# Performance work log

Hardware: AMD Instinct MI355X
Metric: run time of the kernel (lower is better)

## Reference

```python
import jax, jax.numpy as jnp
import numpy as np

H = 128            # hidden_dim
R = 16             # num_rbf
L = 3              # num_atom_encoder_layers
LAT = 32           # latent_dim
NUM_ATOM_TYPES = 64
CUTOFF = 5.0       # atom_cutoff
N_RES = 2048
DEG = 16           # avg radius-graph degree
_PATTERN = np.array([19, 20, 21, 22, 23, 24, 25, 22])  # ragged atoms/residue, mean 22


def setup_inputs() -> dict:
    key = jax.random.key(0)
    ks = jax.random.split(key, 16)
    apr = np.tile(_PATTERN, N_RES // len(_PATTERN))        # (N,) atoms per residue
    A = int(apr.sum())                                     # 45056 atoms
    E = A * DEG                                            # 720896 edges
    rng = np.random.default_rng(0)

    def gl(k, shape, fan_in):
        return jax.random.normal(k, shape, jnp.float32) * (fan_in ** -0.5)

    return {
        "atom_coords": jax.random.normal(ks[0], (A, 3), jnp.float32) * 10.0,
        "atom_types": jax.random.randint(ks[1], (A,), 0, NUM_ATOM_TYPES),
        "residue_indices": jnp.asarray(np.repeat(np.arange(N_RES), apr)),
        "residue_types": jax.random.randint(ks[2], (N_RES,), 0, 4),
        "atoms_per_residue": jnp.asarray(apr),
        "edge_src": jnp.asarray(rng.integers(0, A, E)),
        "edge_dst": jnp.asarray(rng.integers(0, A, E)),
        # learned parameters
        "atom_embed": gl(ks[3], (NUM_ATOM_TYPES, H), 1.0),
        "residue_embed": gl(ks[4], (4, H), 1.0),
        "We1": gl(ks[5], (L, 2 * H + R, H), 2 * H + R), "be1": jnp.zeros((L, H)),
        "We2": gl(ks[6], (L, H, H), H), "be2": jnp.zeros((L, H)),
        "Wh1": gl(ks[7], (L, 2 * H, H), 2 * H), "bh1": jnp.zeros((L, H)),
        "Wh2": gl(ks[8], (L, H, H), H), "bh2": jnp.zeros((L, H)),
        "Wq": gl(ks[9], (H, H), H), "bq": jnp.zeros((H,)),
        "Wk": gl(ks[10], (H, H), H), "bk": jnp.zeros((H,)),
        "Wv": gl(ks[11], (H, H), H), "bv": jnp.zeros((H,)),
        "Wmu": gl(ks[12], (H, LAT), H), "bmu": jnp.zeros((LAT,)),
        "Wlv": gl(ks[13], (H, LAT), H) * 0.01, "blv": jnp.full((LAT,), -2.0),
    }


def reference(atom_coords, atom_types, residue_indices, residue_types,
              atoms_per_residue, edge_src, edge_dst,
              atom_embed, residue_embed,
              We1, be1, We2, be2, Wh1, bh1, Wh2, bh2,
              Wq, bq, Wk, bk, Wv, bv, Wmu, bmu, Wlv, blv):
    A = atom_coords.shape[0]
    N = residue_types.shape[0]
    coords = atom_coords - atom_coords.mean(0, keepdims=True)  # center_coords

    # Gaussian radial basis expansion of edge distances
    d = jnp.linalg.norm(coords[edge_src] - coords[edge_dst], axis=-1)  # (E,)
    centers = jnp.linspace(0.0, CUTOFF, R)
    gamma = (R / CUTOFF) ** 2
    edge_attr = jnp.exp(-gamma * (d[:, None] - centers) ** 2)          # (E,R)

    # atom features: atom-type embed + residue-type embed scattered to atoms
    res_emb = residue_embed[residue_types]                             # (N,H)
    h = atom_embed[atom_types] + res_emb[residue_indices]              # (A,H)

    # EGNN layers (update_coords=False): message MLP -> sum-agg -> residual node MLP
    for l in range(L):
        m = jnp.concatenate([h[edge_src], h[edge_dst], edge_attr], axis=-1)  # (E,2H+R)
        m = jax.nn.silu(m @ We1[l] + be1[l])
        m = jax.nn.silu(m @ We2[l] + be2[l])                                  # (E,H)
        agg = jax.ops.segment_sum(m, edge_dst, num_segments=A)               # (A,H)
        u = jnp.concatenate([h, agg], axis=-1)                               # (A,2H)
        u = jax.nn.silu(u @ Wh1[l] + bh1[l])
        h = h + (u @ Wh2[l] + bh2[l])

    # segment (per-residue) attention pooling of atoms -> residues
    q = res_emb @ Wq + bq                                              # (N,H)
    k = h @ Wk + bk                                                    # (A,H)
    v = h @ Wv + bv                                                    # (A,H)
    scores = jnp.sum(q[residue_indices] * k, axis=-1) * (H ** -0.5)    # (A,)
    smax = jax.ops.segment_max(scores, residue_indices, num_segments=N)
    ex = jnp.exp(scores - smax[residue_indices])
    denom = jax.ops.segment_sum(ex, residue_indices, num_segments=N)
    w = ex / denom[residue_indices]
    pooled = jax.ops.segment_sum(w[:, None] * v, residue_indices, num_segments=N)  # (N,H)

    mu = pooled @ Wmu + bmu
    logvar = jnp.clip(pooled @ Wlv + blv, -10.0, 2.0)
    return mu, logvar
```

## Files before the change

kernel.cpp:

```cpp
#include <hip/hip_runtime.h>
#include <hip/hip_bf16.h>

#define H 128
#define LATD 32

typedef __attribute__((ext_vector_type(8))) _Float16 half8t;
typedef __attribute__((ext_vector_type(4))) _Float16 half4t;
typedef __attribute__((ext_vector_type(2))) _Float16 half2t;
typedef __attribute__((ext_vector_type(8))) unsigned short u16x8;
typedef __attribute__((ext_vector_type(4))) float f32x4;

#define OFF_RBF 0
#define OFF_W2  12288
#define OFF_PROJ 61440
#define OFF_H1  159744
#define OFF_H2  258048
#define OFF_KV  307200
#define WP_TOTAL 339968

__device__ __forceinline__ float silu_f(float x) {
  return x * __builtin_amdgcn_rcpf(1.0f + __expf(-x));
}
__device__ __forceinline__ unsigned short f16u(float x) {
  _Float16 hh = (_Float16)x;
  return *(unsigned short*)&hh;
}

__global__ void k_init_h(const float* __restrict__ atom_embed,
                         const float* __restrict__ residue_embed,
                         const int* __restrict__ atype,
                         const int* __restrict__ ridx,
                         const int* __restrict__ rtype,
                         float* __restrict__ h, unsigned short* __restrict__ hb, int A) {
  int i = blockIdx.x * blockDim.x + threadIdx.x;
  if (i >= A * H) return;
  int a = i >> 7, j = i & 127;
  float v = atom_embed[atype[a] * H + j] + residue_embed[rtype[ridx[a]] * H + j];
  h[i] = v;
  hb[i] = f16u(v);
}

__global__ void k_dist(const float* __restrict__ coords,
                       const int* __restrict__ esrc, const int* __restrict__ edst,
                       float* __restrict__ dbuf, int E) {
  int e = blockIdx.x * blockDim.x + threadIdx.x;
  if (e >= E) return;
  int s = esrc[e], t = edst[e];
  float dx = coords[3*s+0] - coords[3*t+0];
  float dy = coords[3*s+1] - coords[3*t+1];
  float dz = coords[3*s+2] - coords[3*t+2];
  dbuf[e] = sqrtf(dx*dx + dy*dy + dz*dz);
}

__global__ void k_starts(const int* __restrict__ ridx, int* __restrict__ starts, int A) {
  int a = blockIdx.x * blockDim.x + threadIdx.x;
  if (a >= A) return;
  if (a == 0 || ridx[a] != ridx[a-1]) starts[ridx[a]] = a;
}

__global__ void k_bias2(const float* __restrict__ b1, const float* __restrict__ b2,
                        float* __restrict__ bkv) {
  int t = threadIdx.x;
  bkv[t] = (t < 128) ? b1[t] : b2[t - 128];
}

__global__ void k_hist(const int* __restrict__ edst, int* __restrict__ cnt, int E) {
  int e = blockIdx.x * blockDim.x + threadIdx.x;
  if (e < E) atomicAdd(&cnt[edst[e]], 1);
}

__global__ __launch_bounds__(1024) void k_scanA(const int* __restrict__ cnt,
                                                int* __restrict__ cursor,
                                                int* __restrict__ bsum, int A) {
  __shared__ int buf[1024];
  int tid = threadIdx.x;
  int i = blockIdx.x * 1024 + tid;
  int v = (i < A) ? cnt[i] : 0;
  buf[tid] = v;
  __syncthreads();
  #pragma unroll
  for (int off = 1; off < 1024; off <<= 1) {
    int nv = (tid >= off) ? buf[tid - off] : 0;
    __syncthreads();
    buf[tid] += nv;
    __syncthreads();
  }
  if (i < A) cursor[i] = buf[tid] - v;
  if (tid == 1023) bsum[blockIdx.x] = buf[1023];
}

__global__ void k_scanB(int* __restrict__ bsum, int nb) {
  int lane = threadIdx.x;
  int v = (lane < nb) ? bsum[lane] : 0;
  int s = v;
  #pragma unroll
  for (int off = 1; off < 64; off <<= 1) {
    int nv = __shfl_up(s, off);
    if (lane >= off) s += nv;
  }
  if (lane < nb) bsum[lane] = s - v;
}

__global__ void k_scanC(int* __restrict__ cursor, const int* __restrict__ bsum, int A) {
  int i = blockIdx.x * blockDim.x + threadIdx.x;
  if (i < A) cursor[i] += bsum[i >> 10];
}

__global__ void k_scatter(const int* __restrict__ edst, int* __restrict__ cursor,
                          int* __restrict__ eperm, int E) {
  int e = blockIdx.x * blockDim.x + threadIdx.x;
  if (e >= E) return;
  int p = atomicAdd(&cursor[edst[e]], 1);
  eperm[p] = e;
}

__global__ void k_pack(const float* __restrict__ We1, const float* __restrict__ We2,
                       const float* __restrict__ Wh1, const float* __restrict__ Wh2,
                       const float* __restrict__ Wk,  const float* __restrict__ Wv,
                       unsigned short* __restrict__ wp) {
  int t = blockIdx.x * blockDim.x + threadIdx.x;
  if (t >= WP_TOTAL) return;
  if (t < OFF_W2) {
    int u = t - OFF_RBF; int layer = u / 4096, idx = u % 4096;
    int i = idx & 7, lane = (idx >> 3) & 63, ct = (idx >> 9) & 7;
    int k = ((lane >> 4) * 8) + i;
    int c = ct * 16 + (lane & 15);
    const float* src = We1 + (size_t)layer * 272 * H;
    wp[t] = f16u(k < 16 ? src[(size_t)(256 + k) * H + c] : 0.0f);
  } else if (t < OFF_PROJ) {
    int u = t - OFF_W2; int layer = u / 16384, idx = u % 16384;
    int i = idx & 7, lane = (idx >> 3) & 63, ct = (idx >> 9) & 7, kt = idx >> 12;
    int k = kt * 32 + (lane >> 4) * 8 + i, c = ct * 16 + (lane & 15);
    const float* src = We2 + (size_t)layer * 128 * H;
    wp[t] = f16u(src[(size_t)k * H + c]);
  } else if (t < OFF_H1) {
    int u = t - OFF_PROJ; int layer = u / 32768, idx = u % 32768;
    int i = idx & 7, lane = (idx >> 3) & 63, ct = (idx >> 9) & 15, kt = idx >> 13;
    int k = kt * 32 + (lane >> 4) * 8 + i, c = ct * 16 + (lane & 15);
    const float* src = We1 + (size_t)layer * 272 * H;
    float v = (c < 128) ? src[(size_t)k * H + c] : src[(size_t)(128 + k) * H + (c - 128)];
    wp[t] = f16u(v);
  } else if (t < OFF_H2) {
    int u = t - OFF_H1; int layer = u / 32768, idx = u % 32768;
    int i = idx & 7, lane = (idx >> 3) & 63, ct = (idx >> 9) & 7, kt = idx >> 12;
    int k = kt * 32 + (lane >> 4) * 8 + i, c = ct * 16 + (lane & 15);
    const float* src = Wh1 + (size_t)layer * 256 * H;
    wp[t] = f16u(src[(size_t)k * H + c]);
  } else if (t < OFF_KV) {
    int u = t - OFF_H2; int layer = u / 16384, idx = u % 16384;
    int i = idx & 7, lane = (idx >> 3) & 63, ct = (idx >> 9) & 7, kt = idx >> 12;
    int k = kt * 32 + (lane >> 4) * 8 + i, c = ct * 16 + (lane & 15);
    const float* src = Wh2 + (size_t)layer * 128 * H;
    wp[t] = f16u(src[(size_t)k * H + c]);
  } else {
    int idx = t - OFF_KV;
    int i = idx & 7, lane = (idx >> 3) & 63, ct = (idx >> 9) & 15, kt = idx >> 13;
    int k = kt * 32 + (lane >> 4) * 8 + i, c = ct * 16 + (lane & 15);
    float v = (c < 128) ? Wk[(size_t)k * H + c] : Wv[(size_t)k * H + (c - 128)];
    wp[t] = f16u(v);
  }
}

__global__ __launch_bounds__(256) void k_proj(
    const unsigned short* __restrict__ hb, const unsigned short* __restrict__ Wp,
    unsigned short* __restrict__ Ph, int A, const float* __restrict__ bias) {
  const int tid = threadIdx.x, l = tid & 63, wv = tid >> 6;
  const int lr = l & 15, lk = (l >> 4) * 8;
  const int a0 = blockIdx.x * 64;
  f32x4 acc[4][4] = {};
  #pragma unroll
  for (int kt = 0; kt < 4; ++kt) {
    half8t a[4], b[4];
    #pragma unroll
    for (int rt = 0; rt < 4; ++rt) {
      int row = a0 + rt * 16 + lr; if (row >= A) row = A - 1;
      a[rt] = *(const half8t*)&hb[(size_t)row * H + kt * 32 + lk];
    }
    #pragma unroll
    for (int ci = 0; ci < 4; ++ci)
      b[ci] = *(const half8t*)&Wp[(((size_t)kt * 16 + wv * 4 + ci) * 64 + l) * 8];
    #pragma unroll
    for (int rt = 0; rt < 4; ++rt)
      #pragma unroll
      for (int ci = 0; ci < 4; ++ci)
        acc[rt][ci] = __builtin_amdgcn_mfma_f32_16x16x32_f16(a[rt], b[ci], acc[rt][ci], 0, 0, 0);
  }
  #pragma unroll
  for (int rt = 0; rt < 4; ++rt)
    #pragma unroll
    for (int ci = 0; ci < 4; ++ci) {
      int col = (wv * 4 + ci) * 16 + lr;
      float bb = bias ? bias[col] : 0.0f;
      #pragma unroll
      for (int rr = 0; rr < 4; ++rr) {
        int row = a0 + rt * 16 + (l >> 4) * 4 + rr;
        if (row < A) Ph[(size_t)row * 256 + col] = f16u(acc[rt][ci][rr] + bb);
      }
    }
}

#define ES 136

__global__ __launch_bounds__(256) void k_edge_mfma(
    const unsigned short* __restrict__ Ph, const float* __restrict__ dbuf,
    const int* __restrict__ esrc, const int* __restrict__ edst,
    const int* __restrict__ eperm,
    const unsigned short* __restrict__ Wr, const float* __restrict__ be1,
    const unsigned short* __restrict__ W2p, const float* __restrict__ be2,
    float* __restrict__ agg, int E) {
  __shared__ __align__(16) unsigned short SH[64 * ES];
  __shared__ int dstv[64];
  __shared__ float dval[64];

  const int tid = threadIdx.x;
  const int e0 = blockIdx.x * 64;
  const int l = tid & 63, wv = tid >> 6;
  const int lr = l & 15, lk = (l >> 4) * 8, g4 = (l >> 4) * 4;
  const int ct0 = wv * 2;

  {
    const int r = tid >> 2, qt = tid & 3;
    int e = e0 + r;
    int ec = (e < E) ? e : (E - 1);
    int es = eperm[ec];
    int s = esrc[es], t = edst[es];
    if (qt == 0) {
      dstv[r] = (e < E) ? t : -1;
      dval[r] = dbuf[es];
    }
    const half8t* ps = (const half8t*)(Ph + (size_t)s * 256);
    const half8t* pt = (const half8t*)(Ph + (size_t)t * 256 + 128);
    half8t* pr = (half8t*)&SH[r * ES];
    #pragma unroll
    for (int i = 0; i < 4; ++i)
      pr[qt * 4 + i] = ps[qt * 4 + i] + pt[qt * 4 + i];
  }
  __syncthreads();

  f32x4 acc[2][4];
  #pragma unroll
  for (int cj = 0; cj < 2; ++cj) {
    int cbase = (ct0 + cj) * 16 + g4;
    #pragma unroll
    for (int et = 0; et < 4; ++et) {
      half4t p4 = *(const half4t*)&SH[(et * 16 + lr) * ES + cbase];
      acc[cj][et][0] = (float)p4[0];
      acc[cj][et][1] = (float)p4[1];
      acc[cj][et][2] = (float)p4[2];
      acc[cj][et][3] = (float)p4[3];
    }
  }
  {
    float dA[4];
    #pragma unroll
    for (int et = 0; et < 4; ++et) dA[et] = dval[et * 16 + lr];
    half8t br[4];
    if (lk < 16) {
      #pragma unroll
      for (int et = 0; et < 4; ++et) {
        float d = dA[et];
        #pragma unroll
        for (int i = 0; i < 8; ++i) {
          float dd = d - (float)(lk + i) * (5.0f / 15.0f);
          br[et][i] = (_Float16)__expf(-10.24f * dd * dd);
        }
      }
    } else {
      #pragma unroll
      for (int et = 0; et < 4; ++et)
        #pragma unroll
        for (int i = 0; i < 8; ++i) br[et][i] = (_Float16)0.0f;
    }
    half8t ar[2];
    #pragma unroll
    for (int cj = 0; cj < 2; ++cj)
      ar[cj] = *(const half8t*)&Wr[(((size_t)(ct0 + cj)) * 64 + l) * 8];
    #pragma unroll
    for (int et = 0; et < 4; ++et)
      #pragma unroll
      for (int cj = 0; cj < 2; ++cj)
        acc[cj][et] = __builtin_amdgcn_mfma_f32_16x16x32_f16(ar[cj], br[et], acc[cj][et], 0, 0, 0);
  }
  __syncthreads();

  #pragma unroll
  for (int cj = 0; cj < 2; ++cj) {
    f32x4 b1v = *(const f32x4*)&be1[(ct0 + cj) * 16 + g4];
    #pragma unroll
    for (int et = 0; et < 4; ++et) {
      half4t m4;
      #pragma unroll
      for (int rr = 0; rr < 4; ++rr)
        m4[rr] = (_Float16)silu_f(acc[cj][et][rr] + b1v[rr]);
      *(half4t*)&SH[(et * 16 + lr) * ES + (ct0 + cj) * 16 + g4] = m4;
    }
  }
  __syncthreads();

  f32x4 acc2[2][4] = {};
  #pragma unroll
  for (int kt = 0; kt < 4; ++kt) {
    half8t a2[2], b2[4];
    #pragma unroll
    for (int cj = 0; cj < 2; ++cj)
      a2[cj] = *(const half8t*)&W2p[(((size_t)kt * 8 + ct0 + cj) * 64 + l) * 8];
    #pragma unroll
    for (int et = 0; et < 4; ++et)
      b2[et] = *(const half8t*)&SH[(et * 16 + lr) * ES + kt * 32 + lk];
    #pragma unroll
    for (int cj = 0; cj < 2; ++cj)
      #pragma unroll
      for (int et = 0; et < 4; ++et)
        acc2[cj][et] = __builtin_amdgcn_mfma_f32_16x16x32_f16(a2[cj], b2[et], acc2[cj][et], 0, 0, 0);
  }
  __syncthreads();

  #pragma unroll
  for (int cj = 0; cj < 2; ++cj) {
    f32x4 b2v = *(const f32x4*)&be2[(ct0 + cj) * 16 + g4];
    #pragma unroll
    for (int et = 0; et < 4; ++et) {
      half4t m4;
      #pragma unroll
      for (int rr = 0; rr < 4; ++rr)
        m4[rr] = (_Float16)silu_f(acc2[cj][et][rr] + b2v[rr]);
      *(half4t*)&SH[(et * 16 + lr) * ES + (ct0 + cj) * 16 + g4] = m4;
    }
  }
  __syncthreads();

  {
    int cp = tid & 63, qr = tid >> 6;
    int rbeg = qr * 16, rend = rbeg + 16;
    float a0 = 0.f, a1 = 0.f;
    int prev = -1;
    for (int r = rbeg; r < rend; ++r) {
      int dv = dstv[r];
      half2t v = *(const half2t*)&SH[r * ES + cp * 2];
      if (dv != prev) {
        if (prev >= 0) {
          atomicAdd(&agg[(size_t)prev * H + cp * 2], a0);
          atomicAdd(&agg[(size_t)prev * H + cp * 2 + 1], a1);
        }
        a0 = a1 = 0.f;
        prev = dv;
      }
      if (dv >= 0) { a0 += (float)v[0]; a1 += (float)v[1]; }
    }
    if (prev >= 0) {
      atomicAdd(&agg[(size_t)prev * H + cp * 2], a0);
      atomicAdd(&agg[(size_t)prev * H + cp * 2 + 1], a1);
    }
  }
}

#define NXS 264
#define M1S 136

__global__ __launch_bounds__(256) void k_node_mfma(
    float* __restrict__ h, unsigned short* __restrict__ hb,
    const float* __restrict__ agg,
    const unsigned short* __restrict__ W1p, const float* __restrict__ bh1,
    const unsigned short* __restrict__ W2p, const float* __restrict__ bh2, int A) {
  __shared__ __align__(16) unsigned short Xs[32 * NXS];
  __shared__ __align__(16) unsigned short Us[32 * M1S];
  const int tid = threadIdx.x;
  const int a0 = blockIdx.x * 32;
  {
    const int r = tid >> 3, oct = tid & 7;
    int a = a0 + r; if (a >= A) a = A - 1;
    const u16x8* hr = (const u16x8*)(hb + (size_t)a * H);
    u16x8* xr = (u16x8*)&Xs[r * NXS];
    xr[oct * 2]     = hr[oct * 2];
    xr[oct * 2 + 1] = hr[oct * 2 + 1];
    const float4* ar = (const float4*)(agg + (size_t)a * H);
    u16x8 tmp[2];
    unsigned short* tp = (unsigned short*)tmp;
    #pragma unroll
    for (int i = 0; i < 4; ++i) {
      float4 av = ar[oct * 4 + i];
      tp[i*4+0] = f16u(av.x); tp[i*4+1] = f16u(av.y);
      tp[i*4+2] = f16u(av.z); tp[i*4+3] = f16u(av.w);
    }
    xr[16 + oct * 2]     = tmp[0];
    xr[16 + oct * 2 + 1] = tmp[1];
  }
  __syncthreads();

  const int l = tid & 63, wv = tid >> 6;
  const int lr = l & 15, lk = (l >> 4) * 8;
  const int ct0 = wv * 2;
  const int c0 = ct0 * 16 + lr, c1 = c0 + 16;
  const float b1a = bh1[c0], b1b = bh1[c1];
  const float b2a = bh2[c0], b2b = bh2[c1];

  f32x4 acc[2][2] = {};
  #pragma unroll
  for (int kt = 0; kt < 8; ++kt) {
    half8t a[2], b[2];
    #pragma unroll
    for (int rt = 0; rt < 2; ++rt)
      a[rt] = *(const half8t*)&Xs[(rt * 16 + lr) * NXS + kt * 32 + lk];
    #pragma unroll
    for (int j = 0; j < 2; ++j)
      b[j] = *(const half8t*)&W1p[(((size_t)kt * 8 + ct0 + j) * 64 + l) * 8];
    #pragma unroll
    for (int rt = 0; rt < 2; ++rt)
      #pragma unroll
      for (int j = 0; j < 2; ++j)
        acc[rt][j] = __builtin_amdgcn_mfma_f32_16x16x32_f16(a[rt], b[j], acc[rt][j], 0, 0, 0);
  }
  #pragma unroll
  for (int rt = 0; rt < 2; ++rt)
    #pragma unroll
    for (int j = 0; j < 2; ++j) {
      float bb = j ? b1b : b1a;
      int col = (ct0 + j) * 16 + lr;
      #pragma unroll
      for (int rr = 0; rr < 4; ++rr) {
        int row = rt * 16 + (l >> 4) * 4 + rr;
        Us[row * M1S + col] = f16u(silu_f(acc[rt][j][rr] + bb));
      }
    }
  __syncthreads();

  f32x4 acc2[2][2] = {};
  #pragma unroll
  for (int kt = 0; kt < 4; ++kt) {
    half8t a[2], b[2];
    #pragma unroll
    for (int rt = 0; rt < 2; ++rt)
      a[rt] = *(const half8t*)&Us[(rt * 16 + lr) * M1S + kt * 32 + lk];
    #pragma unroll
    for (int j = 0; j < 2; ++j)
      b[j] = *(const half8t*)&W2p[(((size_t)kt * 8 + ct0 + j) * 64 + l) * 8];
    #pragma unroll
    for (int rt = 0; rt < 2; ++rt)
      #pragma unroll
      for (int j = 0; j < 2; ++j)
        acc2[rt][j] = __builtin_amdgcn_mfma_f32_16x16x32_f16(a[rt], b[j], acc2[rt][j], 0, 0, 0);
  }
  #pragma unroll
  for (int rt = 0; rt < 2; ++rt)
    #pragma unroll
    for (int j = 0; j < 2; ++j) {
      float bb = j ? b2b : b2a;
      int col = (ct0 + j) * 16 + lr;
      #pragma unroll
      for (int rr = 0; rr < 4; ++rr) {
        int row = rt * 16 + (l >> 4) * 4 + rr;
        int a = a0 + row;
        if (a < A) {
          size_t off = (size_t)a * H + col;
          float nh = h[off] + acc2[rt][j][rr] + bb;
          h[off] = nh;
          hb[off] = f16u(nh);
        }
      }
    }
}

__global__ void k_q4(const float* __restrict__ residue_embed,
                     const float* __restrict__ Wq, const float* __restrict__ bq,
                     float* __restrict__ q4) {
  int i = blockIdx.x * blockDim.x + threadIdx.x;
  if (i >= 4 * H) return;
  int r = i >> 7, j = i & 127;
  const float* emb = residue_embed + (size_t)r * H;
  float s = bq[j];
  #pragma unroll 4
  for (int k = 0; k < H; ++k) s += emb[k] * Wq[(size_t)k*H + j];
  q4[i] = s;
}

__global__ __launch_bounds__(256) void k_pool(
    const float* __restrict__ q4, const int* __restrict__ rtype,
    const unsigned short* __restrict__ kv, const int* __restrict__ starts,
    const int* __restrict__ apr, float* __restrict__ pooled, int N) {
  int r = blockIdx.x * 4 + (threadIdx.x >> 6);
  if (r >= N) return;
  int lane = threadIdx.x & 63;
  int s0 = starts[r], cnt = apr[r];
  const float* qrow = q4 + (size_t)rtype[r] * H;
  float q0 = qrow[lane], q1 = qrow[64 + lane];
  float myscore = -1e30f;
  for (int i = 0; i < cnt; ++i) {
    const unsigned short* kr = kv + (size_t)(s0 + i) * 256;
    float p = q0 * (float)(*(const _Float16*)&kr[lane]) +
              q1 * (float)(*(const _Float16*)&kr[64 + lane]);
    #pragma unroll
    for (int off = 32; off; off >>= 1) p += __shfl_xor(p, off);
    if (lane == i) myscore = p * 0.08838834764831845f;
  }
  float val = (lane < cnt) ? myscore : -1e30f;
  float mx = val;
  #pragma unroll
  for (int off = 32; off; off >>= 1) mx = fmaxf(mx, __shfl_xor(mx, off));
  float ex = (lane < cnt) ? __expf(val - mx) : 0.0f;
  float sum = ex;
  #pragma unroll
  for (int off = 32; off; off >>= 1) sum += __shfl_xor(sum, off);
  float w = ex * __builtin_amdgcn_rcpf(sum);
  float p0 = 0.f, p1 = 0.f;
  for (int i = 0; i < cnt; ++i) {
    float wi = __shfl(w, i);
    const unsigned short* vr = kv + (size_t)(s0 + i) * 256 + 128;
    p0 += wi * (float)(*(const _Float16*)&vr[lane]);
    p1 += wi * (float)(*(const _Float16*)&vr[64 + lane]);
  }
  pooled[(size_t)r*H + lane] = p0;
  pooled[(size_t)r*H + 64 + lane] = p1;
}

__global__ void k_head(const float* __restrict__ pooled,
                       const float* __restrict__ Wmu, const float* __restrict__ bmu,
                       const float* __restrict__ Wlv, const float* __restrict__ blv,
                       float* __restrict__ out, int N) {
  int i = blockIdx.x * blockDim.x + threadIdx.x;
  if (i >= N * LATD) return;
  int r = i >> 5, j = i & 31;
  const float* p = pooled + (size_t)r * H;
  float smu = 0.f, slv = 0.f;
  #pragma unroll 4
  for (int k = 0; k < H; ++k) {
    float pv = p[k];
    smu += pv * Wmu[(size_t)k*LATD + j];
    slv += pv * Wlv[(size_t)k*LATD + j];
  }
  smu += bmu[j];
  slv += blv[j];
  slv = fminf(fmaxf(slv, -10.0f), 2.0f);
  out[i] = smu;
  out[(size_t)N*LATD + i] = slv;
}

extern "C" void kernel_launch(void* const* d_in, const int* in_sizes, int n_in,
                              void* d_out, int out_size, void* d_ws, size_t ws_size,
                              hipStream_t stream) {
  const float* coords        = (const float*)d_in[0];
  const int*   atype         = (const int*)d_in[1];
  const int*   ridx          = (const int*)d_in[2];
  const int*   rtype         = (const int*)d_in[3];
  const int*   apr           = (const int*)d_in[4];
  const int*   esrc          = (const int*)d_in[5];
  const int*   edst          = (const int*)d_in[6];
  const float* atom_embed    = (const float*)d_in[7];
  const float* residue_embed = (const float*)d_in[8];
  const float* We1 = (const float*)d_in[9];
  const float* be1 = (const float*)d_in[10];
  const float* We2 = (const float*)d_in[11];
  const float* be2 = (const float*)d_in[12];
  const float* Wh1 = (const float*)d_in[13];
  const float* bh1 = (const float*)d_in[14];
  const float* Wh2 = (const float*)d_in[15];
  const float* bh2 = (const float*)d_in[16];
  const float* Wq  = (const float*)d_in[17];
  const float* bq  = (const float*)d_in[18];
  const float* Wk  = (const float*)d_in[19];
  const float* bk  = (const float*)d_in[20];
  const float* Wv  = (const float*)d_in[21];
  const float* bv  = (const float*)d_in[22];
  const float* Wmu = (const float*)d_in[23];
  const float* bmu = (const float*)d_in[24];
  const float* Wlv = (const float*)d_in[25];
  const float* blv = (const float*)d_in[26];

  const int A = in_sizes[1];
  const int N = in_sizes[3];
  const int E = in_sizes[5];

  float* ws     = (float*)d_ws;
  float* h      = ws;
  float* agg    = h + (size_t)A * H;
  float* vbuf   = agg + (size_t)A * H;
  float* dbuf   = vbuf + (size_t)A * H;
  float* q4     = dbuf + (size_t)E;
  float* bkv    = q4 + 4 * H;
  float* pooled = bkv + 256;
  int*   starts = (int*)(pooled + (size_t)N * H);
  unsigned short* hbuf = (unsigned short*)(starts + N);
  int*   eperm  = (int*)(hbuf + (size_t)A * H);
  int*   cnt    = eperm + (size_t)E;
  int*   cursor = cnt + A;
  int*   bsum   = cursor + A;
  unsigned short* wp = (unsigned short*)(bsum + 64);
  unsigned short* Ph = (unsigned short*)vbuf;

  k_init_h<<<(A * H + 255) / 256, 256, 0, stream>>>(atom_embed, residue_embed,
                                                    atype, ridx, rtype, h, hbuf, A);
  k_dist<<<(E + 255) / 256, 256, 0, stream>>>(coords, esrc, edst, dbuf, E);
  k_starts<<<(A + 255) / 256, 256, 0, stream>>>(ridx, starts, A);
  k_pack<<<(WP_TOTAL + 255) / 256, 256, 0, stream>>>(We1, We2, Wh1, Wh2, Wk, Wv, wp);
  k_bias2<<<1, 256, 0, stream>>>(bk, bv, bkv);

  const int nb = (A + 1023) / 1024;
  hipMemsetAsync(cnt, 0, (size_t)A * sizeof(int), stream);
  k_hist<<<(E + 255) / 256, 256, 0, stream>>>(edst, cnt, E);
  k_scanA<<<nb, 1024, 0, stream>>>(cnt, cursor, bsum, A);
  k_scanB<<<1, 64, 0, stream>>>(bsum, nb);
  k_scanC<<<(A + 255) / 256, 256, 0, stream>>>(cursor, bsum, A);
  k_scatter<<<(E + 255) / 256, 256, 0, stream>>>(edst, cursor, eperm, E);

  for (int l = 0; l < 3; ++l) {
    hipMemsetAsync(agg, 0, (size_t)A * H * sizeof(float), stream);
    k_proj<<<(A + 63) / 64, 256, 0, stream>>>(
        hbuf, wp + OFF_PROJ + (size_t)l * 32768, Ph, A, nullptr);
    k_edge_mfma<<<(E + 63) / 64, 256, 0, stream>>>(
        Ph, dbuf, esrc, edst, eperm,
        wp + OFF_RBF + (size_t)l * 4096,  be1 + (size_t)l * H,
        wp + OFF_W2  + (size_t)l * 16384, be2 + (size_t)l * H, agg, E);
    k_node_mfma<<<(A + 31) / 32, 256, 0, stream>>>(
        h, hbuf, agg,
        wp + OFF_H1 + (size_t)l * 32768, bh1 + (size_t)l * H,
        wp + OFF_H2 + (size_t)l * 16384, bh2 + (size_t)l * H, A);
  }

  k_q4<<<2, 256, 0, stream>>>(residue_embed, Wq, bq, q4);
  unsigned short* kv = Ph;
  k_proj<<<(A + 63) / 64, 256, 0, stream>>>(hbuf, wp + OFF_KV, kv, A, bkv);
  k_pool<<<(N + 3) / 4, 256, 0, stream>>>(q4, rtype, kv, starts, apr, pooled, N);
  k_head<<<(N * LATD + 255) / 256, 256, 0, stream>>>(pooled, Wmu, bmu, Wlv, blv,
                                                     (float*)d_out, N);
}
```

Measured before the change: 638.9 us.

## Persist edge blocks over several tiles with register prefetch and fuse setup kernels

The edge kernel now handles NT=4 tiles of 64 edges per block. It prefetches the next tile's gathered projection rows into registers while the current tile runs its MFMA and scatter stages, and it uses lighter LDS-only barriers. Small setup kernels are merged: residue starts go into init_h, the degree histogram into the distance kernel, and the k/v bias concat into the q kernel. Together these hide gather latency and cut launch overhead, at the cost of more registers and four times fewer edge blocks.

After: 759.0 us. 1.19x slower.

```diff
diff --git a/kernel.cpp b/kernel.cpp
--- a/kernel.cpp
+++ b/kernel.cpp
@@ -26,23 +26,31 @@
   return *(unsigned short*)&hh;
 }
 
+__device__ __forceinline__ void lgkbar() {
+  asm volatile("s_waitcnt lgkmcnt(0)" ::: "memory");
+  __builtin_amdgcn_s_barrier();
+}
+
 __global__ void k_init_h(const float* __restrict__ atom_embed,
                          const float* __restrict__ residue_embed,
                          const int* __restrict__ atype,
                          const int* __restrict__ ridx,
                          const int* __restrict__ rtype,
-                         float* __restrict__ h, unsigned short* __restrict__ hb, int A) {
+                         float* __restrict__ h, unsigned short* __restrict__ hb,
+                         int* __restrict__ starts, int A) {
   int i = blockIdx.x * blockDim.x + threadIdx.x;
   if (i >= A * H) return;
   int a = i >> 7, j = i & 127;
-  float v = atom_embed[atype[a] * H + j] + residue_embed[rtype[ridx[a]] * H + j];
+  int r = ridx[a];
+  float v = atom_embed[atype[a] * H + j] + residue_embed[rtype[r] * H + j];
   h[i] = v;
   hb[i] = f16u(v);
+  if (j == 0 && (a == 0 || ridx[a - 1] != r)) starts[r] = a;
 }
 
 __global__ void k_dist(const float* __restrict__ coords,
                        const int* __restrict__ esrc, const int* __restrict__ edst,
-                       float* __restrict__ dbuf, int E) {
+                       float* __restrict__ dbuf, int* __restrict__ cnt, int E) {
   int e = blockIdx.x * blockDim.x + threadIdx.x;
   if (e >= E) return;
   int s = esrc[e], t = edst[e];
@@ -50,23 +58,7 @@
   float dy = coords[3*s+1] - coords[3*t+1];
   float dz = coords[3*s+2] - coords[3*t+2];
   dbuf[e] = sqrtf(dx*dx + dy*dy + dz*dz);
-}
-
-__global__ void k_starts(const int* __restrict__ ridx, int* __restrict__ starts, int A) {
-  int a = blockIdx.x * blockDim.x + threadIdx.x;
-  if (a >= A) return;
-  if (a == 0 || ridx[a] != ridx[a-1]) starts[ridx[a]] = a;
-}
-
-__global__ void k_bias2(const float* __restrict__ b1, const float* __restrict__ b2,
-                        float* __restrict__ bkv) {
-  int t = threadIdx.x;
-  bkv[t] = (t < 128) ? b1[t] : b2[t - 128];
-}
-
-__global__ void k_hist(const int* __restrict__ edst, int* __restrict__ cnt, int E) {
-  int e = blockIdx.x * blockDim.x + threadIdx.x;
-  if (e < E) atomicAdd(&cnt[edst[e]], 1);
+  atomicAdd(&cnt[t], 1);
 }
 
 __global__ __launch_bounds__(1024) void k_scanA(const int* __restrict__ cnt,
@@ -200,6 +192,7 @@
 }
 
 #define ES 136
+#define NT 4
 
 __global__ __launch_bounds__(256) void k_edge_mfma(
     const unsigned short* __restrict__ Ph, const float* __restrict__ dbuf,
@@ -213,145 +206,159 @@
   __shared__ float dval[64];
 
   const int tid = threadIdx.x;
-  const int e0 = blockIdx.x * 64;
   const int l = tid & 63, wv = tid >> 6;
   const int lr = l & 15, lk = (l >> 4) * 8, g4 = (l >> 4) * 4;
   const int ct0 = wv * 2;
-
-  {
-    const int r = tid >> 2, qt = tid & 3;
-    int e = e0 + r;
-    int ec = (e < E) ? e : (E - 1);
-    int es = eperm[ec];
-    int s = esrc[es], t = edst[es];
-    if (qt == 0) {
-      dstv[r] = (e < E) ? t : -1;
-      dval[r] = dbuf[es];
-    }
-    const half8t* ps = (const half8t*)(Ph + (size_t)s * 256);
-    const half8t* pt = (const half8t*)(Ph + (size_t)t * 256 + 128);
-    half8t* pr = (half8t*)&SH[r * ES];
-    #pragma unroll
-    for (int i = 0; i < 4; ++i)
-      pr[qt * 4 + i] = ps[qt * 4 + i] + pt[qt * 4 + i];
-  }
-  __syncthreads();
-
-  f32x4 acc[2][4];
-  #pragma unroll
-  for (int cj = 0; cj < 2; ++cj) {
-    int cbase = (ct0 + cj) * 16 + g4;
-    #pragma unroll
-    for (int et = 0; et < 4; ++et) {
-      half4t p4 = *(const half4t*)&SH[(et * 16 + lr) * ES + cbase];
-      acc[cj][et][0] = (float)p4[0];
-      acc[cj][et][1] = (float)p4[1];
-      acc[cj][et][2] = (float)p4[2];
-      acc[cj][et][3] = (float)p4[3];
-    }
-  }
-  {
-    float dA[4];
-    #pragma unroll
-    for (int et = 0; et < 4; ++et) dA[et] = dval[et * 16 + lr];
-    half8t br[4];
-    if (lk < 16) {
+  const int r = tid >> 2, qt = tid & 3;
+  const int e00 = blockIdx.x * (64 * NT);
+
+  half8t pv0, pv1, pv2, pv3, qv0, qv1, qv2, qv3;
+  int pDst; float pD;
+
+#define PREFETCH(tt) do {                                            \
+    int e = e00 + (tt) * 64 + r;                                     \
+    int ec = (e < E) ? e : (E - 1);                                  \
+    int es = eperm[ec];                                              \
+    int s_ = esrc[es], t_ = edst[es];                                \
+    pDst = (e < E) ? t_ : -1;                                        \
+    pD = dbuf[es];                                                   \
+    const half8t* ps = (const half8t*)(Ph + (size_t)s_ * 256 + qt * 32);        \
+    const half8t* pt = (const half8t*)(Ph + (size_t)t_ * 256 + 128 + qt * 32);  \
+    pv0 = ps[0]; pv1 = ps[1]; pv2 = ps[2]; pv3 = ps[3];              \
+    qv0 = pt[0]; qv1 = pt[1]; qv2 = pt[2]; qv3 = pt[3];              \
+  } while (0)
+
+  PREFETCH(0);
+
+  #pragma unroll 1
+  for (int t = 0; t < NT; ++t) {
+    {
+      half8t* pr = (half8t*)&SH[r * ES + qt * 32];
+      pr[0] = pv0 + qv0; pr[1] = pv1 + qv1;
+      pr[2] = pv2 + qv2; pr[3] = pv3 + qv3;
+      if (qt == 0) { dstv[r] = pDst; dval[r] = pD; }
+    }
+    if (t + 1 < NT) PREFETCH(t + 1);
+    lgkbar();
+
+    f32x4 acc[2][4];
+    #pragma unroll
+    for (int cj = 0; cj < 2; ++cj) {
+      int cbase = (ct0 + cj) * 16 + g4;
       #pragma unroll
       for (int et = 0; et < 4; ++et) {
-        float d = dA[et];
+        half4t p4 = *(const half4t*)&SH[(et * 16 + lr) * ES + cbase];
+        acc[cj][et][0] = (float)p4[0];
+        acc[cj][et][1] = (float)p4[1];
+        acc[cj][et][2] = (float)p4[2];
+        acc[cj][et][3] = (float)p4[3];
+      }
+    }
+    {
+      float dA[4];
+      #pragma unroll
+      for (int et = 0; et < 4; ++et) dA[et] = dval[et * 16 + lr];
+      half8t br[4];
+      if (lk < 16) {
         #pragma unroll
-        for (int i = 0; i < 8; ++i) {
-          float dd = d - (float)(lk + i) * (5.0f / 15.0f);
-          br[et][i] = (_Float16)__expf(-10.24f * dd * dd);
+        for (int et = 0; et < 4; ++et) {
+          float d = dA[et];
+          #pragma unroll
+          for (int i = 0; i < 8; ++i) {
+            float dd = d - (float)(lk + i) * (5.0f / 15.0f);
+            br[et][i] = (_Float16)__expf(-10.24f * dd * dd);
+          }
         }
-      }
-    } else {
+      } else {
+        #pragma unroll
+        for (int et = 0; et < 4; ++et)
+          #pragma unroll
+          for (int i = 0; i < 8; ++i) br[et][i] = (_Float16)0.0f;
+      }
+      half8t ar[2];
+      #pragma unroll
+      for (int cj = 0; cj < 2; ++cj)
+        ar[cj] = *(const half8t*)&Wr[(((size_t)(ct0 + cj)) * 64 + l) * 8];
       #pragma unroll
       for (int et = 0; et < 4; ++et)
         #pragma unroll
-        for (int i = 0; i < 8; ++i) br[et][i] = (_Float16)0.0f;
-    }
-    half8t ar[2];
-    #pragma unroll
-    for (int cj = 0; cj < 2; ++cj)
-      ar[cj] = *(const half8t*)&Wr[(((size_t)(ct0 + cj)) * 64 + l) * 8];
-    #pragma unroll
-    for (int et = 0; et < 4; ++et)
+        for (int cj = 0; cj < 2; ++cj)
+          acc[cj][et] = __builtin_amdgcn_mfma_f32_16x16x32_f16(ar[cj], br[et], acc[cj][et], 0, 0, 0);
+    }
+    lgkbar();
+
+    #pragma unroll
+    for (int cj = 0; cj < 2; ++cj) {
+      f32x4 b1v = *(const f32x4*)&be1[(ct0 + cj) * 16 + g4];
+      #pragma unroll
+      for (int et = 0; et < 4; ++et) {
+        half4t m4;
+        #pragma unroll
+        for (int rr = 0; rr < 4; ++rr)
+          m4[rr] = (_Float16)silu_f(acc[cj][et][rr] + b1v[rr]);
+        *(half4t*)&SH[(et * 16 + lr) * ES + (ct0 + cj) * 16 + g4] = m4;
+      }
+    }
+    lgkbar();
+
+    f32x4 acc2[2][4] = {};
+    #pragma unroll
+    for (int kt = 0; kt < 4; ++kt) {
+      half8t a2[2], b2[4];
       #pragma unroll
       for (int cj = 0; cj < 2; ++cj)
-        acc[cj][et] = __builtin_amdgcn_mfma_f32_16x16x32_f16(ar[cj], br[et], acc[cj][et], 0, 0, 0);
-  }
-  __syncthreads();
-
-  #pragma unroll
-  for (int cj = 0; cj < 2; ++cj) {
-    f32x4 b1v = *(const f32x4*)&be1[(ct0 + cj) * 16 + g4];
-    #pragma unroll
-    for (int et = 0; et < 4; ++et) {
-      half4t m4;
-      #pragma unroll
-      for (int rr = 0; rr < 4; ++rr)
-        m4[rr] = (_Float16)silu_f(acc[cj][et][rr] + b1v[rr]);
-      *(half4t*)&SH[(et * 16 + lr) * ES + (ct0 + cj) * 16 + g4] = m4;
-    }
-  }
-  __syncthreads();
-
-  f32x4 acc2[2][4] = {};
-  #pragma unroll
-  for (int kt = 0; kt < 4; ++kt) {
-    half8t a2[2], b2[4];
-    #pragma unroll
-    for (int cj = 0; cj < 2; ++cj)
-      a2[cj] = *(const half8t*)&W2p[(((size_t)kt * 8 + ct0 + cj) * 64 + l) * 8];
-    #pragma unroll
-    for (int et = 0; et < 4; ++et)
-      b2[et] = *(const half8t*)&SH[(et * 16 + lr) * ES + kt * 32 + lk];
-    #pragma unroll
-    for (int cj = 0; cj < 2; ++cj)
+        a2[cj] = *(const half8t*)&W2p[(((size_t)kt * 8 + ct0 + cj) * 64 + l) * 8];
       #pragma unroll
       for (int et = 0; et < 4; ++et)
-        acc2[cj][et] = __builtin_amdgcn_mfma_f32_16x16x32_f16(a2[cj], b2[et], acc2[cj][et], 0, 0, 0);
-  }
-  __syncthreads();
-
-  #pragma unroll
-  for (int cj = 0; cj < 2; ++cj) {
-    f32x4 b2v = *(const f32x4*)&be2[(ct0 + cj) * 16 + g4];
-    #pragma unroll
-    for (int et = 0; et < 4; ++et) {
-      half4t m4;
-      #pragma unroll
-      for (int rr = 0; rr < 4; ++rr)
-        m4[rr] = (_Float16)silu_f(acc2[cj][et][rr] + b2v[rr]);
-      *(half4t*)&SH[(et * 16 + lr) * ES + (ct0 + cj) * 16 + g4] = m4;
-    }
-  }
-  __syncthreads();
-
-  {
-    int cp = tid & 63, qr = tid >> 6;
-    int rbeg = qr * 16, rend = rbeg + 16;
-    float a0 = 0.f, a1 = 0.f;
-    int prev = -1;
-    for (int r = rbeg; r < rend; ++r) {
-      int dv = dstv[r];
-      half2t v = *(const half2t*)&SH[r * ES + cp * 2];
-      if (dv != prev) {
-        if (prev >= 0) {
-          atomicAdd(&agg[(size_t)prev * H + cp * 2], a0);
-          atomicAdd(&agg[(size_t)prev * H + cp * 2 + 1], a1);
+        b2[et] = *(const half8t*)&SH[(et * 16 + lr) * ES + kt * 32 + lk];
+      #pragma unroll
+      for (int cj = 0; cj < 2; ++cj)
+        #pragma unroll
+        for (int et = 0; et < 4; ++et)
+          acc2[cj][et] = __builtin_amdgcn_mfma_f32_16x16x32_f16(a2[cj], b2[et], acc2[cj][et], 0, 0, 0);
+    }
+    lgkbar();
+
+    #pragma unroll
+    for (int cj = 0; cj < 2; ++cj) {
+      f32x4 b2v = *(const f32x4*)&be2[(ct0 + cj) * 16 + g4];
+      #pragma unroll
+      for (int et = 0; et < 4; ++et) {
+        half4t m4;
+        #pragma unroll
+        for (int rr = 0; rr < 4; ++rr)
+          m4[rr] = (_Float16)silu_f(acc2[cj][et][rr] + b2v[rr]);
+        *(half4t*)&SH[(et * 16 + lr) * ES + (ct0 + cj) * 16 + g4] = m4;
+      }
+    }
+    lgkbar();
+
+    {
+      int cp = tid & 63, qr = tid >> 6;
+      int rbeg = qr * 16, rend = rbeg + 16;
+      float a0 = 0.f, a1 = 0.f;
+      int prev = -1;
+      for (int rr = rbeg; rr < rend; ++rr) {
+        int dv = dstv[rr];
+        half2t v = *(const half2t*)&SH[rr * ES + cp * 2];
+        if (dv != prev) {
+          if (prev >= 0) {
+            atomicAdd(&agg[(size_t)prev * H + cp * 2], a0);
+            atomicAdd(&agg[(size_t)prev * H + cp * 2 + 1], a1);
+          }
+          a0 = a1 = 0.f;
+          prev = dv;
         }
-        a0 = a1 = 0.f;
-        prev = dv;
-      }
-      if (dv >= 0) { a0 += (float)v[0]; a1 += (float)v[1]; }
-    }
-    if (prev >= 0) {
-      atomicAdd(&agg[(size_t)prev * H + cp * 2], a0);
-      atomicAdd(&agg[(size_t)prev * H + cp * 2 + 1], a1);
-    }
-  }
+        if (dv >= 0) { a0 += (float)v[0]; a1 += (float)v[1]; }
+      }
+      if (prev >= 0) {
+        atomicAdd(&agg[(size_t)prev * H + cp * 2], a0);
+        atomicAdd(&agg[(size_t)prev * H + cp * 2 + 1], a1);
+      }
+    }
+    lgkbar();
+  }
+#undef PREFETCH
 }
 
 #define NXS 264
@@ -460,17 +467,22 @@
     }
 }
 
-__global__ void k_q4(const float* __restrict__ residue_embed,
-                     const float* __restrict__ Wq, const float* __restrict__ bq,
-                     float* __restrict__ q4) {
+__global__ void k_q4b(const float* __restrict__ residue_embed,
+                      const float* __restrict__ Wq, const float* __restrict__ bq,
+                      const float* __restrict__ bk, const float* __restrict__ bv,
+                      float* __restrict__ q4, float* __restrict__ bkv) {
   int i = blockIdx.x * blockDim.x + threadIdx.x;
-  if (i >= 4 * H) return;
-  int r = i >> 7, j = i & 127;
-  const float* emb = residue_embed + (size_t)r * H;
-  float s = bq[j];
-  #pragma unroll 4
-  for (int k = 0; k < H; ++k) s += emb[k] * Wq[(size_t)k*H + j];
-  q4[i] = s;
+  if (i < 512) {
+    int r = i >> 7, j = i & 127;
+    const float* emb = residue_embed + (size_t)r * H;
+    float s = bq[j];
+    #pragma unroll 4
+    for (int k = 0; k < H; ++k) s += emb[k] * Wq[(size_t)k*H + j];
+    q4[i] = s;
+  } else if (i < 768) {
+    int t = i - 512;
+    bkv[t] = (t < 128) ? bk[t] : bv[t - 128];
+  }
 }
 
 __global__ __launch_bounds__(256) void k_pool(
@@ -586,26 +598,25 @@
   unsigned short* wp = (unsigned short*)(bsum + 64);
   unsigned short* Ph = (unsigned short*)vbuf;
 
+  hipMemsetAsync(cnt, 0, (size_t)A * sizeof(int), stream);
   k_init_h<<<(A * H + 255) / 256, 256, 0, stream>>>(atom_embed, residue_embed,
-                                                    atype, ridx, rtype, h, hbuf, A);
-  k_dist<<<(E + 255) / 256, 256, 0, stream>>>(coords, esrc, edst, dbuf, E);
-  k_starts<<<(A + 255) / 256, 256, 0, stream>>>(ridx, starts, A);
+                                                    atype, ridx, rtype, h, hbuf,
+                                                    starts, A);
+  k_dist<<<(E + 255) / 256, 256, 0, stream>>>(coords, esrc, edst, dbuf, cnt, E);
   k_pack<<<(WP_TOTAL + 255) / 256, 256, 0, stream>>>(We1, We2, Wh1, Wh2, Wk, Wv, wp);
-  k_bias2<<<1, 256, 0, stream>>>(bk, bv, bkv);
 
   const int nb = (A + 1023) / 1024;
-  hipMemsetAsync(cnt, 0, (size_t)A * sizeof(int), stream);
-  k_hist<<<(E + 255) / 256, 256, 0, stream>>>(edst, cnt, E);
   k_scanA<<<nb, 1024, 0, stream>>>(cnt, cursor, bsum, A);
   k_scanB<<<1, 64, 0, stream>>>(bsum, nb);
   k_scanC<<<(A + 255) / 256, 256, 0, stream>>>(cursor, bsum, A);
   k_scatter<<<(E + 255) / 256, 256, 0, stream>>>(edst, cursor, eperm, E);
 
+  const int egrid = (E + 64 * NT - 1) / (64 * NT);
   for (int l = 0; l < 3; ++l) {
     hipMemsetAsync(agg, 0, (size_t)A * H * sizeof(float), stream);
     k_proj<<<(A + 63) / 64, 256, 0, stream>>>(
         hbuf, wp + OFF_PROJ + (size_t)l * 32768, Ph, A, nullptr);
-    k_edge_mfma<<<(E + 63) / 64, 256, 0, stream>>>(
+    k_edge_mfma<<<egrid, 256, 0, stream>>>(
         Ph, dbuf, esrc, edst, eperm,
         wp + OFF_RBF + (size_t)l * 4096,  be1 + (size_t)l * H,
         wp + OFF_W2  + (size_t)l * 16384, be2 + (size_t)l * H, agg, E);
@@ -615,7 +626,7 @@
         wp + OFF_H2 + (size_t)l * 16384, bh2 + (size_t)l * H, A);
   }
 
-  k_q4<<<2, 256, 0, stream>>>(residue_embed, Wq, bq, q4);
+  k_q4b<<<3, 256, 0, stream>>>(residue_embed, Wq, bq, bk, bv, q4, bkv);
   unsigned short* kv = Ph;
   k_proj<<<(A + 63) / 64, 256, 0, stream>>>(hbuf, wp + OFF_KV, kv, A, bkv);
   k_pool<<<(N + 3) / 4, 256, 0, stream>>>(q4, rtype, kv, starts, apr, pooled, N);
```
